# Kernel tuning notes

Measured on AMD Instinct MI355X. Metric: run time of the kernel, lower is better.

Reference implementation:

```python
import jax, jax.numpy as jnp
import numpy as np

K = 128      # knowledge_n
E = 4096     # exer_n
S = 2048     # student_n
M = 512      # number of supervised exercises (ex_id)
NUM_UPDATE = 3
THRESHOLD = 0.05
H = 1.0


def setup_inputs() -> dict:
    key = jax.random.key(0)
    ks = jax.random.split(key, 16)
    U_embeding = jax.random.uniform(ks[0], (S, K), dtype=jnp.float32)
    W = jax.random.uniform(ks[1], (K, E), dtype=jnp.float32)
    beiTa_1 = jax.random.uniform(ks[2], (K, E), dtype=jnp.float32)
    beiTa_2 = jax.random.uniform(ks[3], (E, 1), dtype=jnp.float32)
    B = jax.random.uniform(ks[4], (K, E, K), dtype=jnp.float32)
    guess_slip = jax.random.normal(ks[5], (E, 2), dtype=jnp.float32)
    A_emb = jax.random.normal(ks[6], (E, 3), dtype=jnp.float32)
    gamma_c = jax.random.normal(ks[7], (E, 1), dtype=jnp.float32)
    gamma_e = jax.random.normal(ks[8], (E, 1), dtype=jnp.float32)
    alpha = jax.random.normal(ks[9], (E, 1), dtype=jnp.float32)
    score = jax.random.randint(ks[10], (E, 1), 0, 2).astype(jnp.float32)
    user_k_kc = (jax.random.uniform(ks[11], (K, E)) < 0.3).astype(jnp.float32)
    # multi-hot question->concept map, ~4 concepts per exercise, at least 1
    q_kn = (jax.random.uniform(ks[12], (E, K)) < 4.0 / K).astype(jnp.float32)
    q_kn = q_kn.at[jnp.arange(E), jax.random.randint(ks[13], (E,), 0, K)].set(1.0)
    d = q_kn.sum(axis=1, keepdims=True)  # exercise degree, >= 1
    ex_id = jax.random.randint(ks[14], (M,), 0, E, dtype=jnp.int32)
    kn_id = jnp.arange(K, dtype=jnp.int32)
    stu_id = 7
    return dict(U_embeding=U_embeding, W=W, beiTa_1=beiTa_1, beiTa_2=beiTa_2,
                B=B, guess_slip=guess_slip, A_emb=A_emb, gamma_c=gamma_c,
                gamma_e=gamma_e, alpha=alpha, score=score, user_k_kc=user_k_kc,
                q_kn=q_kn, d=d, stu_id=stu_id, kn_id=kn_id, ex_id=ex_id)


def reference(U_embeding, W, beiTa_1, beiTa_2, B, guess_slip, A_emb,
              gamma_c, gamma_e, alpha, score, user_k_kc, q_kn, d,
              stu_id, kn_id, ex_id):
    # The torch loop `for cur_kn in kn_id: update(cur_kn, U_update[num-1])` is a
    # Jacobi sweep: every concept update reads the PREVIOUS state, so all
    # concepts can be computed in one vectorized pass per iteration.
    Bdiag = jnp.einsum('kek->ke', B)           # B[k, e, k], (K, E)
    dvec = d[:, 0]                              # (E,)
    sc = score[:, 0]                            # (E,)
    upd = jnp.zeros((K,), dtype=bool).at[kn_id].set(True)

    def step(u):                                # u: (K,) current mastery state
        # ---- Ic (eq. 7): per-exercise interaction term ----
        su = q_kn @ u                           # (E,)  sum of mastered concepts
        yc = jnp.exp(-(sc - su / dvec) ** 2)    # (E,)
        Pc = jnp.concatenate([1.0 - guess_slip, yc[:, None]], axis=1)  # (E,3)
        Ic = jax.nn.sigmoid(-jnp.sum(A_emb * Pc, axis=1))              # (E,)
        # ---- Gkc: masked, dead-zoned neighbour influence ----
        # U_gkc entries with q_kn==0 are set to 0.5, and column cur_kn is
        # zeroed; dead-zone of 0.5 contributes 0, so it reduces to a gated
        # product with the k-diagonal term subtracted out.
        dv = jnp.where(jnp.abs(u - 0.5) > THRESHOLD, u - 0.5, 0.0)      # (K,)
        qdv = q_kn * dv                         # (E, K)
        Gsum = jnp.einsum('kej,ej->ke', B, qdv) - Bdiag * qdv.T         # (K, E)
        # NOTE: the original subtracts 0.5 twice (sigmoid(...) - 0.5 then
        # reshape(...) - 0.5); replicated faithfully.
        Gkc = jax.nn.sigmoid(-Gsum) - 1.0       # (K, E)
        # ---- Zc ----
        Zc = jax.nn.sigmoid(-(gamma_c[:, 0] / dvec) * (sc - 0.5)) - 0.5  # (E,)
        # ---- WKC and the per-concept contraction over the exercise set ----
        WK = H * Ic[None, :] * (beiTa_1 * Gkc + (beiTa_2[:, 0] * Zc)[None, :])
        s = jnp.sum(user_k_kc * W * WK, axis=1)  # ragged set via 0/1 mask, (K,)
        u_new = jax.nn.sigmoid(-s)
        return jnp.where(upd, u_new, u)

    u0 = U_embeding[stu_id]                     # (K,)
    states = [u0]
    diffs = []
    for _ in range(NUM_UPDATE):
        un = step(states[-1])
        diffs.append(jnp.linalg.norm(un - states[-1]))
        states.append(un)

    state_last = states[-1][:, None]            # U_update[-2] in torch indexing
    state_2nd_last = states[-2][:, None]        # U_update[-3]
    diff_norm = jnp.stack(diffs)

    # ---- supervised predict ----
    Ukse = (q_kn[ex_id] @ state_last) / d[ex_id] - 0.5                  # (M,1)
    predict = jax.nn.sigmoid(-(alpha[ex_id] * Ukse + gamma_e[ex_id]))   # (M,1)
    return (state_last, state_2nd_last, predict, diff_norm)
```

## Files before the change

### kernel.cpp

```cpp
#include <hip/hip_runtime.h>
#include <math.h>

#define KK 128
#define EE 4096
#define MM 512
#define CP 32

#define OFF_U    0
#define OFF_P    128
#define OFF_CNT  2176
#define OFF_IDX  6272
#define OFF_IDXT 137344
#define OFF_PE   268416
#define OFF_GW   288896
#define OFF_HW   813184
#define OFF_BC   1337472

__global__ __launch_bounds__(256) void k_setup(
    const float* __restrict__ U, const float* __restrict__ W,
    const float* __restrict__ beiTa_1, const float* __restrict__ beiTa_2,
    const float* __restrict__ guess_slip, const float* __restrict__ A_emb,
    const float* __restrict__ gamma_c, const float* __restrict__ score,
    const float* __restrict__ ukc, const float* __restrict__ q_kn,
    const float* __restrict__ d, const int* __restrict__ stu_id,
    float* __restrict__ ws)
{
    int tid = threadIdx.x;
    int blk = blockIdx.x;
    if (blk < 16) {
        int e = blk * 256 + tid;
        int* cnt  = (int*)(ws + OFF_CNT);
        int* idx  = (int*)(ws + OFF_IDX);
        int* idxT = (int*)(ws + OFF_IDXT);
        float* P01  = ws + OFF_PE;
        float* a2   = P01 + EE;
        float* scv  = a2 + EE;
        float* invd = scv + EE;
        float* bz   = invd + EE;

        int4 s4 = make_int4(255, 255, 255, 255);
        for (int i4 = 0; i4 < CP / 4; i4++) ((int4*)(idx + e * CP))[i4] = s4;
        const float4* qrow = (const float4*)(q_kn + (size_t)e * KK);
        int c = 0;
        for (int j4 = 0; j4 < KK / 4; j4++) {
            float4 q = qrow[j4];
            int j = j4 * 4;
            if (q.x > 0.5f) { if (c < CP) { idx[e*CP+c] = j;   idxT[c*EE+e] = j;   } c++; }
            if (q.y > 0.5f) { if (c < CP) { idx[e*CP+c] = j+1; idxT[c*EE+e] = j+1; } c++; }
            if (q.z > 0.5f) { if (c < CP) { idx[e*CP+c] = j+2; idxT[c*EE+e] = j+2; } c++; }
            if (q.w > 0.5f) { if (c < CP) { idx[e*CP+c] = j+3; idxT[c*EE+e] = j+3; } c++; }
        }
        c = (c < CP) ? c : CP;
        cnt[e] = c;

        float id_ = 1.0f / d[e];
        invd[e] = id_;
        float scr = score[e];
        scv[e] = scr;
        P01[e] = A_emb[3*e] * (1.0f - guess_slip[2*e]) +
                 A_emb[3*e+1] * (1.0f - guess_slip[2*e+1]);
        a2[e] = A_emb[3*e+2];
        float zc = 1.0f / (1.0f + __expf(gamma_c[e] * id_ * (scr - 0.5f))) - 0.5f;
        bz[e] = beiTa_2[e] * zc;

        if (blk == 0 && tid < KK) ws[tid] = U[(size_t)stu_id[0] * KK + tid];
    } else {
        float* gW = ws + OFF_GW;
        float* hW = ws + OFF_HW;
        int stride = (gridDim.x - 16) * 256;
        for (int t = (blk - 16) * 256 + tid; t < KK * EE; t += stride) {
            float uw = ukc[t] * W[t];
            hW[t] = uw;
            gW[t] = uw * beiTa_1[t];
        }
    }
}

__global__ __launch_bounds__(256) void k_compact(const float* __restrict__ B,
                                                 float* __restrict__ ws)
{
    __shared__ float srow[4][KK];
    int tid  = threadIdx.x;
    int wid  = tid >> 6;
    int lane = tid & 63;
    int w  = blockIdx.x * 4 + wid;
    int k  = w >> 5;
    int ec = w & 31;
    const int* idx = (const int*)(ws + OFF_IDX);
    float* Bc = ws + OFF_BC;
    float* sr = srow[wid];

    int ebase = ec * 128;
    const float2* Brow = (const float2*)(B + ((size_t)k * EE + ebase) * KK);
    for (int t = 0; t < 128; t++) {
        int e = ebase + t;
        float2 v = Brow[(size_t)t * (KK / 2) + lane];
        int j = (lane < CP) ? idx[e * CP + lane] : 255;
        ((float2*)sr)[lane] = v;
        if (j < KK) {
            float val = sr[j];
            Bc[((size_t)k * CP + lane) * EE + e] = val;
        }
    }
}

__global__ __launch_bounds__(256) void k_sparse(float* __restrict__ ws)
{
    __shared__ float lu[KK];
    __shared__ float sdv[KK];
    __shared__ float red[256];
    int tid = threadIdx.x;
    int ec = blockIdx.x;
    int k  = blockIdx.y;
    int e  = ec * 256 + tid;

    if (tid < KK) {
        float uv = ws[tid];
        lu[tid] = uv;
        float t = uv - 0.5f;
        sdv[tid] = (fabsf(t) > 0.05f) ? t : 0.0f;
    }
    __syncthreads();

    const int* cnt    = (const int*)(ws + OFF_CNT);
    const int* idxT   = (const int*)(ws + OFF_IDXT);
    const float* P01  = ws + OFF_PE;
    const float* a2   = P01 + EE;
    const float* scv  = a2 + EE;
    const float* invd = scv + EE;
    const float* bzv  = invd + EE;
    const float* gW   = ws + OFF_GW;
    const float* hW   = ws + OFF_HW;
    const float* Bc   = ws + OFF_BC;

    int c = cnt[e];
    float su = 0.0f, gs = 0.0f;
    for (int i = 0; i < c; i++) {
        int j   = idxT[i * EE + e];
        float b = Bc[((size_t)k * CP + i) * EE + e];
        su += lu[j];
        gs += (j != k) ? b * sdv[j] : 0.0f;
    }
    float t0 = scv[e] - su * invd[e];
    float yc = __expf(-t0 * t0);
    float Ic = 1.0f / (1.0f + __expf(P01[e] + a2[e] * yc));
    float Gkc = 1.0f / (1.0f + __expf(gs)) - 1.0f;
    size_t o = (size_t)k * EE + e;
    float contrib = Ic * (gW[o] * Gkc + hW[o] * bzv[e]);

    red[tid] = contrib;
    __syncthreads();
    for (int s2 = 128; s2 > 0; s2 >>= 1) {
        if (tid < s2) red[tid] += red[tid + s2];
        __syncthreads();
    }
    if (tid == 0) ws[OFF_P + k * 16 + ec] = red[0];
}

__global__ __launch_bounds__(128) void k_update(float* __restrict__ ws,
                                                float* __restrict__ out, int iter)
{
    __shared__ float red[KK];
    int k = threadIdx.x;
    float s = 0.0f;
    const float* p = ws + OFF_P + k * 16;
    for (int t = 0; t < 16; t++) s += p[t];
    float un = 1.0f / (1.0f + __expf(s));
    float uo = ws[k];
    float dd = un - uo;
    red[k] = dd * dd;
    __syncthreads();
    for (int s2 = 64; s2 > 0; s2 >>= 1) {
        if (k < s2) red[k] += red[k + s2];
        __syncthreads();
    }
    if (k == 0) out[768 + iter] = sqrtf(red[0]);
    ws[k] = un;
    if (iter == 1) out[128 + k] = un;
}

__global__ __launch_bounds__(512) void k_final(
    float* __restrict__ ws, float* __restrict__ out,
    const int* __restrict__ ex_id, const float* __restrict__ alpha,
    const float* __restrict__ gamma_e)
{
    __shared__ float un_s[KK];
    __shared__ float red[KK];
    int tid = threadIdx.x;
    if (tid < KK) {
        float s = 0.0f;
        const float* p = ws + OFF_P + tid * 16;
        for (int t = 0; t < 16; t++) s += p[t];
        float un = 1.0f / (1.0f + __expf(s));
        float uo = ws[tid];
        float dd = un - uo;
        red[tid] = dd * dd;
        un_s[tid] = un;
        out[tid] = un;
    }
    __syncthreads();
    for (int s2 = 64; s2 > 0; s2 >>= 1) {
        if (tid < s2) red[tid] += red[tid + s2];
        __syncthreads();
    }
    if (tid == 0) out[770] = sqrtf(red[0]);

    const int* cnt = (const int*)(ws + OFF_CNT);
    const int* idx = (const int*)(ws + OFF_IDX);
    const float* invd = ws + OFF_PE + 3 * EE;
    int e = ex_id[tid];
    int c = cnt[e];
    const int* ip = idx + e * CP;
    float su = 0.0f;
    for (int i = 0; i < c; i++) su += un_s[ip[i]];
    float Ukse = su * invd[e] - 0.5f;
    out[256 + tid] = 1.0f / (1.0f + __expf(alpha[e] * Ukse + gamma_e[e]));
}

extern "C" void kernel_launch(void* const* d_in, const int* in_sizes, int n_in,
                              void* d_out, int out_size, void* d_ws, size_t ws_size,
                              hipStream_t stream) {
    const float* U          = (const float*)d_in[0];
    const float* W          = (const float*)d_in[1];
    const float* beiTa_1    = (const float*)d_in[2];
    const float* beiTa_2    = (const float*)d_in[3];
    const float* B          = (const float*)d_in[4];
    const float* guess_slip = (const float*)d_in[5];
    const float* A_emb      = (const float*)d_in[6];
    const float* gamma_c    = (const float*)d_in[7];
    const float* gamma_e    = (const float*)d_in[8];
    const float* alpha      = (const float*)d_in[9];
    const float* score      = (const float*)d_in[10];
    const float* ukc        = (const float*)d_in[11];
    const float* q_kn       = (const float*)d_in[12];
    const float* d          = (const float*)d_in[13];
    const int*   stu_id     = (const int*)d_in[14];
    const int*   ex_id      = (const int*)d_in[16];
    float* out = (float*)d_out;
    float* ws  = (float*)d_ws;

    k_setup<<<144, 256, 0, stream>>>(U, W, beiTa_1, beiTa_2, guess_slip, A_emb,
                                     gamma_c, score, ukc, q_kn, d, stu_id, ws);
    k_compact<<<1024, 256, 0, stream>>>(B, ws);
    k_sparse<<<dim3(16, 128), 256, 0, stream>>>(ws);
    k_update<<<1, 128, 0, stream>>>(ws, out, 0);
    k_sparse<<<dim3(16, 128), 256, 0, stream>>>(ws);
    k_update<<<1, 128, 0, stream>>>(ws, out, 1);
    k_sparse<<<dim3(16, 128), 256, 0, stream>>>(ws);
    k_final<<<1, 512, 0, stream>>>(ws, out, ex_id, alpha, gamma_e);
}
```

Measured before the change: 493.0 us.

## Gather only needed B entries and fold state update into the sweep kernel

The B compaction kernel no longer streams every row of B through shared memory. Each thread now gathers only the handful of B[k,e,j] entries named by that exercise's concept list, which cuts the bytes read from the 256 MB B tensor at the cost of scattered, uncoalesced loads. Concept indices are stored as int8 to shrink index traffic. The separate per-iteration update kernels are removed: each sweep kernel recomputes the new state from the previous partial sums, and one block writes the diff norm. Partial sums are double-buffered, and the block reduction now uses wavefront shuffles.

```diff
diff --git a/kernel.cpp b/kernel.cpp
--- a/kernel.cpp
+++ b/kernel.cpp
@@ -7,14 +7,15 @@
 #define CP 32
 
 #define OFF_U    0
-#define OFF_P    128
-#define OFF_CNT  2176
-#define OFF_IDX  6272
-#define OFF_IDXT 137344
-#define OFF_PE   268416
-#define OFF_GW   288896
-#define OFF_HW   813184
-#define OFF_BC   1337472
+#define OFF_PA   128
+#define OFF_PB   2176
+#define OFF_CNT  4224
+#define OFF_IDX  8320
+#define OFF_IDXT 41088
+#define OFF_PE   73856
+#define OFF_GW   94336
+#define OFF_HW   618624
+#define OFF_BC   1142912
 
 __global__ __launch_bounds__(256) void k_setup(
     const float* __restrict__ U, const float* __restrict__ W,
@@ -29,29 +30,31 @@
     int blk = blockIdx.x;
     if (blk < 16) {
         int e = blk * 256 + tid;
-        int* cnt  = (int*)(ws + OFF_CNT);
-        int* idx  = (int*)(ws + OFF_IDX);
-        int* idxT = (int*)(ws + OFF_IDXT);
+        int* cnt = (int*)(ws + OFF_CNT);
+        signed char* idx  = (signed char*)(ws + OFF_IDX);
+        signed char* idxT = (signed char*)(ws + OFF_IDXT);
         float* P01  = ws + OFF_PE;
         float* a2   = P01 + EE;
         float* scv  = a2 + EE;
         float* invd = scv + EE;
         float* bz   = invd + EE;
 
-        int4 s4 = make_int4(255, 255, 255, 255);
-        for (int i4 = 0; i4 < CP / 4; i4++) ((int4*)(idx + e * CP))[i4] = s4;
+        int* ip32 = (int*)(idx + e * CP);
+        #pragma unroll
+        for (int t = 0; t < CP / 4; t++) ip32[t] = -1;
         const float4* qrow = (const float4*)(q_kn + (size_t)e * KK);
         int c = 0;
         for (int j4 = 0; j4 < KK / 4; j4++) {
             float4 q = qrow[j4];
             int j = j4 * 4;
-            if (q.x > 0.5f) { if (c < CP) { idx[e*CP+c] = j;   idxT[c*EE+e] = j;   } c++; }
-            if (q.y > 0.5f) { if (c < CP) { idx[e*CP+c] = j+1; idxT[c*EE+e] = j+1; } c++; }
-            if (q.z > 0.5f) { if (c < CP) { idx[e*CP+c] = j+2; idxT[c*EE+e] = j+2; } c++; }
-            if (q.w > 0.5f) { if (c < CP) { idx[e*CP+c] = j+3; idxT[c*EE+e] = j+3; } c++; }
+            if (q.x > 0.5f) { if (c < CP) idx[e*CP+c] = (signed char)j;     c++; }
+            if (q.y > 0.5f) { if (c < CP) idx[e*CP+c] = (signed char)(j+1); c++; }
+            if (q.z > 0.5f) { if (c < CP) idx[e*CP+c] = (signed char)(j+2); c++; }
+            if (q.w > 0.5f) { if (c < CP) idx[e*CP+c] = (signed char)(j+3); c++; }
         }
         c = (c < CP) ? c : CP;
         cnt[e] = c;
+        for (int i = 0; i < CP; i++) idxT[(size_t)i * EE + e] = idx[e * CP + i];
 
         float id_ = 1.0f / d[e];
         invd[e] = id_;
@@ -67,7 +70,7 @@
     } else {
         float* gW = ws + OFF_GW;
         float* hW = ws + OFF_HW;
-        int stride = (gridDim.x - 16) * 256;
+        int stride = 128 * 256;
         for (int t = (blk - 16) * 256 + tid; t < KK * EE; t += stride) {
             float uw = ukc[t] * W[t];
             hW[t] = uw;
@@ -79,51 +82,53 @@
 __global__ __launch_bounds__(256) void k_compact(const float* __restrict__ B,
                                                  float* __restrict__ ws)
 {
-    __shared__ float srow[4][KK];
-    int tid  = threadIdx.x;
-    int wid  = tid >> 6;
-    int lane = tid & 63;
-    int w  = blockIdx.x * 4 + wid;
-    int k  = w >> 5;
-    int ec = w & 31;
-    const int* idx = (const int*)(ws + OFF_IDX);
-    float* Bc = ws + OFF_BC;
-    float* sr = srow[wid];
-
-    int ebase = ec * 128;
-    const float2* Brow = (const float2*)(B + ((size_t)k * EE + ebase) * KK);
-    for (int t = 0; t < 128; t++) {
-        int e = ebase + t;
-        float2 v = Brow[(size_t)t * (KK / 2) + lane];
-        int j = (lane < CP) ? idx[e * CP + lane] : 255;
-        ((float2*)sr)[lane] = v;
-        if (j < KK) {
-            float val = sr[j];
-            Bc[((size_t)k * CP + lane) * EE + e] = val;
-        }
-    }
-}
-
-__global__ __launch_bounds__(256) void k_sparse(float* __restrict__ ws)
+    int tid = threadIdx.x;
+    int k = blockIdx.y;
+    int e = blockIdx.x * 256 + tid;
+    const signed char* idxT = (const signed char*)(ws + OFF_IDXT);
+    const float* Brow = B + ((size_t)k * EE + e) * KK;
+    float* Bc = ws + OFF_BC + (size_t)k * CP * EE + e;
+
+    for (int i = 0; i < CP; i++) {
+        int j = idxT[(size_t)i * EE + e];
+        unsigned long long m = __ballot(j >= 0);
+        if (!m) break;
+        if (j >= 0) Bc[(size_t)i * EE] = Brow[j];
+    }
+}
+
+__global__ __launch_bounds__(256) void k_phase(
+    float* __restrict__ ws, float* __restrict__ out,
+    const float* __restrict__ pin, float* __restrict__ pout, int phase)
 {
     __shared__ float lu[KK];
     __shared__ float sdv[KK];
-    __shared__ float red[256];
+    __shared__ float red2[KK];
+    __shared__ float wred[4];
     int tid = threadIdx.x;
     int ec = blockIdx.x;
     int k  = blockIdx.y;
     int e  = ec * 256 + tid;
 
     if (tid < KK) {
-        float uv = ws[tid];
+        float uv;
+        if (phase == 0) {
+            uv = ws[tid];
+        } else {
+            float s = 0.0f;
+            const float* p = pin + tid * 16;
+            #pragma unroll
+            for (int t = 0; t < 16; t++) s += p[t];
+            uv = 1.0f / (1.0f + __expf(s));
+        }
         lu[tid] = uv;
         float t = uv - 0.5f;
         sdv[tid] = (fabsf(t) > 0.05f) ? t : 0.0f;
     }
     __syncthreads();
 
-    const int* cnt    = (const int*)(ws + OFF_CNT);
-    const int* idxT   = (const int*)(ws + OFF_IDXT);
+    const int* cnt = (const int*)(ws + OFF_CNT);
+    const signed char* idxT = (const signed char*)(ws + OFF_IDXT);
     const float* P01  = ws + OFF_PE;
     const float* a2   = P01 + EE;
     const float* scv  = a2 + EE;
@@ -134,53 +139,48 @@
     const float* Bc   = ws + OFF_BC;
 
     int c = cnt[e];
+    const signed char* it = idxT + e;
+    const float* bp = Bc + (size_t)k * CP * EE + e;
     float su = 0.0f, gs = 0.0f;
     for (int i = 0; i < c; i++) {
-        int j   = idxT[i * EE + e];
-        float b = Bc[((size_t)k * CP + i) * EE + e];
+        int j   = it[(size_t)i * EE];
+        float b = bp[(size_t)i * EE];
         su += lu[j];
-        gs += (j != k) ? b * sdv[j] : 0.0f;
+        gs = fmaf(b, (j != k) ? sdv[j] : 0.0f, gs);
     }
     float t0 = scv[e] - su * invd[e];
     float yc = __expf(-t0 * t0);
     float Ic = 1.0f / (1.0f + __expf(P01[e] + a2[e] * yc));
     float Gkc = 1.0f / (1.0f + __expf(gs)) - 1.0f;
     size_t o = (size_t)k * EE + e;
-    float contrib = Ic * (gW[o] * Gkc + hW[o] * bzv[e]);
-
-    red[tid] = contrib;
+    float v = Ic * (gW[o] * Gkc + hW[o] * bzv[e]);
+
+    #pragma unroll
+    for (int m = 1; m < 64; m <<= 1) v += __shfl_xor(v, m);
+    if ((tid & 63) == 0) wred[tid >> 6] = v;
     __syncthreads();
-    for (int s2 = 128; s2 > 0; s2 >>= 1) {
-        if (tid < s2) red[tid] += red[tid + s2];
+    if (tid == 0) pout[k * 16 + ec] = wred[0] + wred[1] + wred[2] + wred[3];
+
+    if (phase >= 1 && blockIdx.x == 0 && blockIdx.y == 0) {
+        if (tid < KK) {
+            float dd = lu[tid] - ws[tid];
+            red2[tid] = dd * dd;
+        }
         __syncthreads();
-    }
-    if (tid == 0) ws[OFF_P + k * 16 + ec] = red[0];
-}
-
-__global__ __launch_bounds__(128) void k_update(float* __restrict__ ws,
-                                                float* __restrict__ out, int iter)
-{
-    __shared__ float red[KK];
-    int k = threadIdx.x;
-    float s = 0.0f;
-    const float* p = ws + OFF_P + k * 16;
-    for (int t = 0; t < 16; t++) s += p[t];
-    float un = 1.0f / (1.0f + __expf(s));
-    float uo = ws[k];
-    float dd = un - uo;
-    red[k] = dd * dd;
-    __syncthreads();
-    for (int s2 = 64; s2 > 0; s2 >>= 1) {
-        if (k < s2) red[k] += red[k + s2];
-        __syncthreads();
-    }
-    if (k == 0) out[768 + iter] = sqrtf(red[0]);
-    ws[k] = un;
-    if (iter == 1) out[128 + k] = un;
+        for (int s2 = 64; s2 > 0; s2 >>= 1) {
+            if (tid < s2) red2[tid] += red2[tid + s2];
+            __syncthreads();
+        }
+        if (tid == 0) out[768 + (phase - 1)] = sqrtf(red2[0]);
+        if (tid < KK) {
+            ws[tid] = lu[tid];
+            if (phase == 2) out[128 + tid] = lu[tid];
+        }
+    }
 }
 
 __global__ __launch_bounds__(512) void k_final(
-    float* __restrict__ ws, float* __restrict__ out,
+    float* __restrict__ ws, float* __restrict__ out, const float* __restrict__ pin,
     const int* __restrict__ ex_id, const float* __restrict__ alpha,
     const float* __restrict__ gamma_e)
 {
@@ -189,11 +189,11 @@
     int tid = threadIdx.x;
     if (tid < KK) {
         float s = 0.0f;
-        const float* p = ws + OFF_P + tid * 16;
+        const float* p = pin + tid * 16;
+        #pragma unroll
         for (int t = 0; t < 16; t++) s += p[t];
         float un = 1.0f / (1.0f + __expf(s));
-        float uo = ws[tid];
-        float dd = un - uo;
+        float dd = un - ws[tid];
         red[tid] = dd * dd;
         un_s[tid] = un;
         out[tid] = un;
@@ -206,11 +206,11 @@
     if (tid == 0) out[770] = sqrtf(red[0]);
 
     const int* cnt = (const int*)(ws + OFF_CNT);
-    const int* idx = (const int*)(ws + OFF_IDX);
+    const signed char* idx = (const signed char*)(ws + OFF_IDX);
     const float* invd = ws + OFF_PE + 3 * EE;
     int e = ex_id[tid];
     int c = cnt[e];
-    const int* ip = idx + e * CP;
+    const signed char* ip = idx + (size_t)e * CP;
     float su = 0.0f;
     for (int i = 0; i < c; i++) su += un_s[ip[i]];
     float Ukse = su * invd[e] - 0.5f;
@@ -238,14 +238,14 @@
     const int*   ex_id      = (const int*)d_in[16];
     float* out = (float*)d_out;
     float* ws  = (float*)d_ws;
+    float* pA = ws + OFF_PA;
+    float* pB = ws + OFF_PB;
 
     k_setup<<<144, 256, 0, stream>>>(U, W, beiTa_1, beiTa_2, guess_slip, A_emb,
                                      gamma_c, score, ukc, q_kn, d, stu_id, ws);
-    k_compact<<<1024, 256, 0, stream>>>(B, ws);
-    k_sparse<<<dim3(16, 128), 256, 0, stream>>>(ws);
-    k_update<<<1, 128, 0, stream>>>(ws, out, 0);
-    k_sparse<<<dim3(16, 128), 256, 0, stream>>>(ws);
-    k_update<<<1, 128, 0, stream>>>(ws, out, 1);
-    k_sparse<<<dim3(16, 128), 256, 0, stream>>>(ws);
-    k_final<<<1, 512, 0, stream>>>(ws, out, ex_id, alpha, gamma_e);
-}
+    k_compact<<<dim3(16, 128), 256, 0, stream>>>(B, ws);
+    k_phase<<<dim3(16, 128), 256, 0, stream>>>(ws, out, pA, pA, 0);
+    k_phase<<<dim3(16, 128), 256, 0, stream>>>(ws, out, pA, pB, 1);
+    k_phase<<<dim3(16, 128), 256, 0, stream>>>(ws, out, pB, pA, 2);
+    k_final<<<1, 512, 0, stream>>>(ws, out, pA, ex_id, alpha, gamma_e);
+}
```

Measured after the change: 437.8 us. 1.13x faster.
